# Performance work log

Measured on AMD Instinct MI355X. Metric: run time of the kernel, lower is better.

Reference implementation:

```python
import jax, jax.numpy as jnp
import numpy as np

NUM_HEADS = 16
EMBED = 1024
N, S = 4, 2048


def setup_inputs() -> dict:
    key = jax.random.key(0)
    k1, k2, k3, k4, k5 = jax.random.split(key, 5)
    return {
        "values": jax.random.normal(k1, (N, S, EMBED), dtype=jnp.float32),
        "keys": jax.random.normal(k2, (N, S, EMBED), dtype=jnp.float32),
        "query": jax.random.normal(k3, (N, S, EMBED), dtype=jnp.float32),
        "mask": jnp.ones((N, 1, 1, S), dtype=jnp.int32),
        "W_out": jax.random.normal(k4, (EMBED, EMBED), dtype=jnp.float32) * 0.02,
        "b_out": jax.random.normal(k5, (EMBED,), dtype=jnp.float32) * 0.02,
    }


def reference(values, keys, query, mask, W_out, b_out):
    n, q_len, e = query.shape
    h = NUM_HEADS
    d = e // h
    v = values.reshape(n, -1, h, d)   # [N, K, H, D]
    k = keys.reshape(n, -1, h, d)     # [N, K, H, D]
    q = query.reshape(n, q_len, h, d) # [N, Q, H, D]
    # [N, H, Q, K] similarity (full materialization, as in source)
    sim = jnp.einsum('nqhd,nkhd->nhqk', q, k)
    sim = jnp.where(mask == 0, -jnp.inf, sim)
    # NOTE: source scales by sqrt(embed_size), not sqrt(head_dim)
    attn = jax.nn.softmax(sim / jnp.sqrt(jnp.float32(e)), axis=3)
    out = jnp.einsum('nhqk,nkhd->nqhd', attn, v).reshape(n, q_len, e)
    return out @ W_out.T + b_out
```

## Files before the change

kernel.cpp:

```cpp
#include <hip/hip_runtime.h>

#define SEQ 2048
#define EMBED 1024
#define NHEADS 16
#define HD 64

typedef __attribute__((ext_vector_type(4))) float f32x4;
typedef __attribute__((ext_vector_type(16))) float f32x16;
typedef __attribute__((ext_vector_type(8))) unsigned short u16x8;
typedef __attribute__((ext_vector_type(8))) __bf16 bf16x8;

static __device__ __forceinline__ unsigned cvtpk(float a, float b) {
  unsigned r;
  asm("v_cvt_pk_bf16_f32 %0, %1, %2" : "=v"(r) : "v"(a), "v"(b));
  return r;
}

static __device__ __forceinline__ f32x4 mfma16(u16x8 a, u16x8 b, f32x4 c) {
  return __builtin_amdgcn_mfma_f32_16x16x32_bf16(
      __builtin_bit_cast(bf16x8, a), __builtin_bit_cast(bf16x8, b), c, 0, 0, 0);
}

static __device__ __forceinline__ f32x16 mfma32(u16x8 a, u16x8 b, f32x16 c) {
  return __builtin_amdgcn_mfma_f32_32x32x16_bf16(
      __builtin_bit_cast(bf16x8, a), __builtin_bit_cast(bf16x8, b), c, 0, 0, 0);
}

static __device__ __forceinline__ void gload_lds16(const void* g, void* l) {
  __builtin_amdgcn_global_load_lds(
      (const __attribute__((address_space(1))) unsigned*)g,
      (__attribute__((address_space(3))) unsigned*)l, 16, 0, 0);
}

static __device__ __forceinline__ f32x16 zero16() {
  f32x16 z;
#pragma unroll
  for (int i = 0; i < 16; ++i) z[i] = 0.f;
  return z;
}

static __device__ __forceinline__ u16x8 packfrag(float p0, float p1, float p2, float p3,
                                                 float p4, float p5, float p6, float p7) {
  unsigned L0 = cvtpk(p0, p1);
  unsigned L1 = cvtpk(p2, p3);
  unsigned M0 = cvtpk(p4, p5);
  unsigned M1 = cvtpk(p6, p7);
  asm volatile("v_permlane32_swap_b32 %0, %1" : "+v"(L0), "+v"(M0));
  asm volatile("v_permlane32_swap_b32 %0, %1" : "+v"(L1), "+v"(M1));
  const uint4 fr = make_uint4(L0, L1, M0, M1);
  return __builtin_bit_cast(u16x8, fr);
}

__global__ void convw(const float* __restrict__ W, unsigned short* __restrict__ Wb) {
  const int i = (blockIdx.x * 256 + threadIdx.x) * 4;
  f32x4 v = *(const f32x4*)(W + i);
  *(uint2*)&Wb[i] = make_uint2(cvtpk(v[0], v[1]), cvtpk(v[2], v[3]));
}

__global__ __launch_bounds__(256) void convkv(const float* __restrict__ Kg,
                                              const float* __restrict__ Vg,
                                              unsigned short* __restrict__ Kb,
                                              unsigned short* __restrict__ Vt) {
  const int t = threadIdx.x;
  const int kb = blockIdx.x, nh = blockIdx.y;
  const int n = nh >> 4, h = nh & 15;

  {
    const int k = t >> 2;
    const int ks = t & 3;
    const float* src = Kg + (size_t)(n * SEQ + kb * 64 + k) * EMBED + h * HD + ks * 16;
    f32x4 a = *(const f32x4*)(src);
    f32x4 b = *(const f32x4*)(src + 4);
    f32x4 c = *(const f32x4*)(src + 8);
    f32x4 d = *(const f32x4*)(src + 12);
    unsigned short* dst = Kb + ((size_t)nh * 32 + kb) * 4096 + ks * 1024 + k * 16;
    *(uint4*)&dst[0] =
        make_uint4(cvtpk(a[0], a[1]), cvtpk(a[2], a[3]), cvtpk(b[0], b[1]), cvtpk(b[2], b[3]));
    *(uint4*)&dst[8] =
        make_uint4(cvtpk(c[0], c[1]), cvtpk(c[2], c[3]), cvtpk(d[0], d[1]), cvtpk(d[2], d[3]));
  }

  {
    const int kq = t >> 4, dq = t & 15;
    const int d0 = dq * 4;
    f32x4 vv[4];
#pragma unroll
    for (int i = 0; i < 4; ++i)
      vv[i] = *(const f32x4*)(Vg + (size_t)(n * SEQ + kb * 64 + 4 * kq + i) * EMBED +
                              h * HD + d0);
    unsigned short* dst =
        Vt + ((size_t)nh * 32 + kb) * 4096 + (kq >> 1) * 512 + 4 * (kq & 1);
#pragma unroll
    for (int dj = 0; dj < 4; ++dj) {
      const int d = d0 + dj;
      *(uint2*)&dst[d * 8] =
          make_uint2(cvtpk(vv[0][dj], vv[1][dj]), cvtpk(vv[2][dj], vv[3][dj]));
    }
  }
}

__global__ __launch_bounds__(256, 2) void attn_fused(
    const unsigned short* __restrict__ Kb, const unsigned short* __restrict__ Vtb,
    const float* __restrict__ Qg, const int* __restrict__ maskg,
    unsigned short* __restrict__ attn_out)
{
  __shared__ __align__(16) unsigned short smem[16384];

  const int tid = threadIdx.x;
  const int w = tid >> 6;
  const int l = tid & 63;
  const int q = l & 31;
  const int hi = l >> 5;
  const int id = blockIdx.x;
  const int nh = (id & 7) * 8 + ((id >> 3) & 7);
  const int qb = id >> 6;
  const int n = nh >> 4, h = nh & 15;

  const unsigned short* ksrc = Kb + (size_t)nh * 32 * 4096;
  const unsigned short* vsrc = Vtb + (size_t)nh * 32 * 4096;

  {
    const unsigned short* kg = ksrc + tid * 8;
    const unsigned short* vg = vsrc + tid * 8;
    gload_lds16(kg, &smem[tid * 8]); gload_lds16(kg + 2048, &smem[tid * 8 + 2048]);
    gload_lds16(vg, &smem[8192 + tid * 8]); gload_lds16(vg + 2048, &smem[8192 + tid * 8 + 2048]);
  }

  const float C = 0.04508422f;
  u16x8 qfA[4], qfB[4];
  {
    const float* qp =
        Qg + (size_t)(n * SEQ + qb * 256 + w * 64 + q) * EMBED + h * HD + hi * 8;
#pragma unroll
    for (int ks = 0; ks < 4; ++ks) {
      f32x4 a = *(const f32x4*)(qp + ks * 16);
      f32x4 b = *(const f32x4*)(qp + ks * 16 + 4);
      uint4 pk = make_uint4(cvtpk(a[0] * C, a[1] * C), cvtpk(a[2] * C, a[3] * C),
                            cvtpk(b[0] * C, b[1] * C), cvtpk(b[2] * C, b[3] * C));
      qfA[ks] = __builtin_bit_cast(u16x8, pk);
      f32x4 a2 = *(const f32x4*)(qp + 32 * EMBED + ks * 16);
      f32x4 b2 = *(const f32x4*)(qp + 32 * EMBED + ks * 16 + 4);
      uint4 pk2 = make_uint4(cvtpk(a2[0] * C, a2[1] * C), cvtpk(a2[2] * C, a2[3] * C),
                             cvtpk(b2[0] * C, b2[1] * C), cvtpk(b2[2] * C, b2[3] * C));
      qfB[ks] = __builtin_bit_cast(u16x8, pk2);
    }
  }

  const uint4 onesu = make_uint4(0x3F803F80u, 0x3F803F80u, 0x3F803F80u, 0x3F803F80u);
  const u16x8 ones = __builtin_bit_cast(u16x8, onesu);

  f32x16 o0A = zero16(), o1A = zero16(), o0B = zero16(), o1B = zero16();
  f32x16 laccA = zero16(), laccB = zero16();
  const int kA = q * 16 + hi * 8;
  const int vA = q * 8 + hi * 512;

#pragma unroll 1
  for (int kb = 0; kb < 32; ++kb) {
    const int kbase = (kb & 1) << 12;
    const int vbase = 8192 + kbase;
    const int mv = maskg[n * SEQ + kb * 64 + l];
    __syncthreads();
    if (kb < 31) {
      const unsigned short* kg = ksrc + (size_t)(kb + 1) * 4096 + tid * 8;
      const unsigned short* vg = vsrc + (size_t)(kb + 1) * 4096 + tid * 8;
      const int ob = ((kb + 1) & 1) << 12;
      gload_lds16(kg, &smem[ob + tid * 8]);
      gload_lds16(kg + 2048, &smem[ob + tid * 8 + 2048]);
      gload_lds16(vg, &smem[8192 + ob + tid * 8]);
      gload_lds16(vg + 2048, &smem[8192 + ob + tid * 8 + 2048]);
    }
    const bool anym = __any(mv == 0);

    f32x16 sA0 = zero16(), sA1 = zero16(), sB0 = zero16(), sB1 = zero16();
    __builtin_amdgcn_s_setprio(1);
#pragma unroll
    for (int ks = 0; ks < 4; ++ks) {
      u16x8 k0 = *(const u16x8*)&smem[kbase + ks * 1024 + kA];
      sA0 = mfma32(k0, qfA[ks], sA0);
      sB0 = mfma32(k0, qfB[ks], sB0);
      u16x8 k1 = *(const u16x8*)&smem[kbase + ks * 1024 + kA + 512];
      sA1 = mfma32(k1, qfA[ks], sA1);
      sB1 = mfma32(k1, qfB[ks], sB1);
    }
    __builtin_amdgcn_s_setprio(0);

    if (anym) {
#pragma unroll
      for (int r = 0; r < 16; ++r) {
        const int kl = (r & 3) + 8 * (r >> 2) + 4 * hi;
        const float b0 = maskg[n * SEQ + kb * 64 + kl] ? 0.f : -1e5f;
        const float b1 = maskg[n * SEQ + kb * 64 + kl + 32] ? 0.f : -1e5f;
        sA0[r] += b0; sB0[r] += b0;
        sA1[r] += b1; sB1[r] += b1;
      }
    }

#pragma unroll
    for (int r = 0; r < 16; ++r) {
      sA0[r] = __builtin_amdgcn_exp2f(sA0[r]);
      sA1[r] = __builtin_amdgcn_exp2f(sA1[r]);
      sB0[r] = __builtin_amdgcn_exp2f(sB0[r]);
      sB1[r] = __builtin_amdgcn_exp2f(sB1[r]);
    }

    u16x8 paA[4], paB[4];
    paA[0] = packfrag(sA0[0], sA0[1], sA0[2], sA0[3], sA0[4], sA0[5], sA0[6], sA0[7]);
    paA[1] = packfrag(sA0[8], sA0[9], sA0[10], sA0[11], sA0[12], sA0[13], sA0[14], sA0[15]);
    paA[2] = packfrag(sA1[0], sA1[1], sA1[2], sA1[3], sA1[4], sA1[5], sA1[6], sA1[7]);
    paA[3] = packfrag(sA1[8], sA1[9], sA1[10], sA1[11], sA1[12], sA1[13], sA1[14], sA1[15]);
    paB[0] = packfrag(sB0[0], sB0[1], sB0[2], sB0[3], sB0[4], sB0[5], sB0[6], sB0[7]);
    paB[1] = packfrag(sB0[8], sB0[9], sB0[10], sB0[11], sB0[12], sB0[13], sB0[14], sB0[15]);
    paB[2] = packfrag(sB1[0], sB1[1], sB1[2], sB1[3], sB1[4], sB1[5], sB1[6], sB1[7]);
    paB[3] = packfrag(sB1[8], sB1[9], sB1[10], sB1[11], sB1[12], sB1[13], sB1[14], sB1[15]);

    __builtin_amdgcn_s_setprio(1);
#pragma unroll
    for (int idx = 0; idx < 4; ++idx) {
      u16x8 v0 = *(const u16x8*)&smem[vbase + idx * 1024 + vA];
      o0A = mfma32(v0, paA[idx], o0A);
      o0B = mfma32(v0, paB[idx], o0B);
      u16x8 v1 = *(const u16x8*)&smem[vbase + idx * 1024 + vA + 256];
      o1A = mfma32(v1, paA[idx], o1A);
      o1B = mfma32(v1, paB[idx], o1B);
      laccA = mfma32(ones, paA[idx], laccA);
      laccB = mfma32(ones, paB[idx], laccB);
    }
    __builtin_amdgcn_s_setprio(0);
  }

  const float invA = 1.f / laccA[0];
  const float invB = 1.f / laccB[0];
  __syncthreads();
  unsigned short* ep = &smem[w * 2304];
  const size_t orow = (size_t)n * SEQ + qb * 256 + w * 64;

#pragma unroll
  for (int u = 0; u < 4; ++u) {
    *(uint2*)&ep[q * 72 + 8 * u + 4 * hi] =
        make_uint2(cvtpk(o0A[4 * u] * invA, o0A[4 * u + 1] * invA),
                   cvtpk(o0A[4 * u + 2] * invA, o0A[4 * u + 3] * invA));
    *(uint2*)&ep[q * 72 + 8 * u + 4 * hi + 32] =
        make_uint2(cvtpk(o1A[4 * u] * invA, o1A[4 * u + 1] * invA),
                   cvtpk(o1A[4 * u + 2] * invA, o1A[4 * u + 3] * invA));
  }
  asm volatile("s_waitcnt lgkmcnt(0)" ::: "memory");
#pragma unroll
  for (int i = 0; i < 4; ++i) {
    const int q2 = i * 8 + (l >> 3);
    const uint4 vv = *(const uint4*)&ep[q2 * 72 + (l & 7) * 8];
    *(uint4*)&attn_out[(orow + q2) * EMBED + h * HD + (l & 7) * 8] = vv;
  }
  asm volatile("s_waitcnt lgkmcnt(0)" ::: "memory");

#pragma unroll
  for (int u = 0; u < 4; ++u) {
    *(uint2*)&ep[q * 72 + 8 * u + 4 * hi] =
        make_uint2(cvtpk(o0B[4 * u] * invB, o0B[4 * u + 1] * invB),
                   cvtpk(o0B[4 * u + 2] * invB, o0B[4 * u + 3] * invB));
    *(uint2*)&ep[q * 72 + 8 * u + 4 * hi + 32] =
        make_uint2(cvtpk(o1B[4 * u] * invB, o1B[4 * u + 1] * invB),
                   cvtpk(o1B[4 * u + 2] * invB, o1B[4 * u + 3] * invB));
  }
  asm volatile("s_waitcnt lgkmcnt(0)" ::: "memory");
#pragma unroll
  for (int i = 0; i < 4; ++i) {
    const int q2 = i * 8 + (l >> 3);
    const uint4 vv = *(const uint4*)&ep[q2 * 72 + (l & 7) * 8];
    *(uint4*)&attn_out[(orow + 32 + q2) * EMBED + h * HD + (l & 7) * 8] = vv;
  }
}

__global__ __launch_bounds__(256, 2) void proj_gemm(
    const unsigned short* __restrict__ A, const unsigned short* __restrict__ Bw,
    const float* __restrict__ bias, float* __restrict__ out)
{
  __shared__ __align__(16) unsigned short As[128 * 64];
  __shared__ __align__(16) unsigned short Bs[128 * 64];
  const int tid = threadIdx.x;
  const int l = tid & 63, m = l & 15, g = l >> 4;
  const int w = tid >> 6, wm = w >> 1, wn = w & 1;
  const int m0 = blockIdx.y * 128, n0 = blockIdx.x * 128;
  const int srow = tid >> 3, slot = tid & 7;

  f32x4 acc[4][4];
#pragma unroll
  for (int i = 0; i < 4; ++i)
#pragma unroll
    for (int j = 0; j < 4; ++j) acc[i][j] = (f32x4){0.f, 0.f, 0.f, 0.f};

  for (int kk = 0; kk < EMBED; kk += 64) {
    __syncthreads();
#pragma unroll
    for (int i = 0; i < 4; ++i) {
      const int row = i * 32 + srow;
      u16x8 va = *(const u16x8*)(A + (size_t)(m0 + row) * EMBED + kk + slot * 8);
      u16x8 vb = *(const u16x8*)(Bw + (size_t)(n0 + row) * EMBED + kk + slot * 8);
      const int soff = (slot * 8) ^ ((row & 7) << 3);
      *(u16x8*)&As[row * 64 + soff] = va;
      *(u16x8*)&Bs[row * 64 + soff] = vb;
    }
    __syncthreads();
#pragma unroll
    for (int kc = 0; kc < 2; ++kc) {
      u16x8 af[4], bf[4];
#pragma unroll
      for (int mi = 0; mi < 4; ++mi) {
        const int row = wm * 64 + mi * 16 + m;
        af[mi] = *(const u16x8*)&As[row * 64 + ((kc * 32 + g * 8) ^ ((row & 7) << 3))];
      }
#pragma unroll
      for (int ni = 0; ni < 4; ++ni) {
        const int row = wn * 64 + ni * 16 + m;
        bf[ni] = *(const u16x8*)&Bs[row * 64 + ((kc * 32 + g * 8) ^ ((row & 7) << 3))];
      }
#pragma unroll
      for (int mi = 0; mi < 4; ++mi)
#pragma unroll
        for (int ni = 0; ni < 4; ++ni)
          acc[mi][ni] = mfma16(af[mi], bf[ni], acc[mi][ni]);
    }
  }

#pragma unroll
  for (int ni = 0; ni < 4; ++ni) {
    const int col = n0 + wn * 64 + ni * 16 + m;
    const float bv = bias[col];
#pragma unroll
    for (int mi = 0; mi < 4; ++mi) {
      const int rb = m0 + wm * 64 + mi * 16 + g * 4;
#pragma unroll
      for (int r = 0; r < 4; ++r)
        out[(size_t)(rb + r) * EMBED + col] = acc[mi][ni][r] + bv;
    }
  }
}

extern "C" void kernel_launch(void* const* d_in, const int* in_sizes, int n_in,
                              void* d_out, int out_size, void* d_ws, size_t ws_size,
                              hipStream_t stream) {
  const float* Vg = (const float*)d_in[0];
  const float* Kg = (const float*)d_in[1];
  const float* Qg = (const float*)d_in[2];
  const int* maskg = (const int*)d_in[3];
  const float* Wg = (const float*)d_in[4];
  const float* bg = (const float*)d_in[5];

  unsigned short* attn = (unsigned short*)d_ws;
  unsigned short* Wb = attn + (size_t)4 * SEQ * EMBED;
  unsigned short* Kb = Wb + (size_t)EMBED * EMBED;
  unsigned short* Vt = Kb + (size_t)4 * SEQ * EMBED;
  float* out = (float*)d_out;

  convw<<<dim3(EMBED * EMBED / 1024), 256, 0, stream>>>(Wg, Wb);
  convkv<<<dim3(SEQ / 64, 4 * NHEADS), 256, 0, stream>>>(Kg, Vg, Kb, Vt);
  attn_fused<<<dim3(512), 256, 0, stream>>>(Kb, Vt, Qg, maskg, attn);
  proj_gemm<<<dim3(EMBED / 128, 4 * SEQ / 128), 256, 0, stream>>>(attn, Wb, bg, out);
}
```

Baseline: 130.4 us.

## Fuse weight conversion into KV conversion, precompute mask bias in LDS, tighten loop barriers

```diff
diff --git a/kernel.cpp b/kernel.cpp
--- a/kernel.cpp
+++ b/kernel.cpp
@@ -51,16 +51,12 @@
   return __builtin_bit_cast(u16x8, fr);
 }
 
-__global__ void convw(const float* __restrict__ W, unsigned short* __restrict__ Wb) {
-  const int i = (blockIdx.x * 256 + threadIdx.x) * 4;
-  f32x4 v = *(const f32x4*)(W + i);
-  *(uint2*)&Wb[i] = make_uint2(cvtpk(v[0], v[1]), cvtpk(v[2], v[3]));
-}
-
 __global__ __launch_bounds__(256) void convkv(const float* __restrict__ Kg,
                                               const float* __restrict__ Vg,
+                                              const float* __restrict__ Wg,
                                               unsigned short* __restrict__ Kb,
-                                              unsigned short* __restrict__ Vt) {
+                                              unsigned short* __restrict__ Vt,
+                                              unsigned short* __restrict__ Wb) {
   const int t = threadIdx.x;
   const int kb = blockIdx.x, nh = blockIdx.y;
   const int n = nh >> 4, h = nh & 15;
@@ -97,6 +93,12 @@
           make_uint2(cvtpk(vv[0][dj], vv[1][dj]), cvtpk(vv[2][dj], vv[3][dj]));
     }
   }
+
+  {
+    const int bid = blockIdx.y * 32 + blockIdx.x;
+    const float2 wv = *(const float2*)&Wg[(size_t)bid * 512 + t * 2];
+    ((unsigned*)Wb)[(size_t)bid * 256 + t] = cvtpk(wv.x, wv.y);
+  }
 }
 
 __global__ __launch_bounds__(256, 2) void attn_fused(
@@ -105,6 +107,8 @@
     unsigned short* __restrict__ attn_out)
 {
   __shared__ __align__(16) unsigned short smem[16384];
+  __shared__ float bias_lds[2048];
+  __shared__ int maskflag;
 
   const int tid = threadIdx.x;
   const int w = tid >> 6;
@@ -118,6 +122,24 @@
 
   const unsigned short* ksrc = Kb + (size_t)nh * 32 * 4096;
   const unsigned short* vsrc = Vtb + (size_t)nh * 32 * 4096;
+
+  if (tid == 0) maskflag = 0;
+  const int4 m4a = *(const int4*)&maskg[n * SEQ + tid * 8];
+  const int4 m4b = *(const int4*)&maskg[n * SEQ + tid * 8 + 4];
+  bias_lds[tid * 8 + 0] = m4a.x ? 0.f : -1e5f;
+  bias_lds[tid * 8 + 1] = m4a.y ? 0.f : -1e5f;
+  bias_lds[tid * 8 + 2] = m4a.z ? 0.f : -1e5f;
+  bias_lds[tid * 8 + 3] = m4a.w ? 0.f : -1e5f;
+  bias_lds[tid * 8 + 4] = m4b.x ? 0.f : -1e5f;
+  bias_lds[tid * 8 + 5] = m4b.y ? 0.f : -1e5f;
+  bias_lds[tid * 8 + 6] = m4b.z ? 0.f : -1e5f;
+  bias_lds[tid * 8 + 7] = m4b.w ? 0.f : -1e5f;
+  __syncthreads();
+  if ((m4a.x == 0) || (m4a.y == 0) || (m4a.z == 0) || (m4a.w == 0) ||
+      (m4b.x == 0) || (m4b.y == 0) || (m4b.z == 0) || (m4b.w == 0))
+    maskflag = 1;
+  __syncthreads();
+  const bool anyz = (maskflag != 0);
 
   {
     const unsigned short* kg = ksrc + tid * 8;
@@ -158,8 +180,6 @@
   for (int kb = 0; kb < 32; ++kb) {
     const int kbase = (kb & 1) << 12;
     const int vbase = 8192 + kbase;
-    const int mv = maskg[n * SEQ + kb * 64 + l];
-    __syncthreads();
     if (kb < 31) {
       const unsigned short* kg = ksrc + (size_t)(kb + 1) * 4096 + tid * 8;
       const unsigned short* vg = vsrc + (size_t)(kb + 1) * 4096 + tid * 8;
@@ -168,8 +188,13 @@
       gload_lds16(kg + 2048, &smem[ob + tid * 8 + 2048]);
       gload_lds16(vg, &smem[8192 + ob + tid * 8]);
       gload_lds16(vg + 2048, &smem[8192 + ob + tid * 8 + 2048]);
-    }
-    const bool anym = __any(mv == 0);
+      asm volatile("s_waitcnt vmcnt(4)" ::: "memory");
+    } else {
+      asm volatile("s_waitcnt vmcnt(0)" ::: "memory");
+    }
+    __builtin_amdgcn_sched_barrier(0);
+    __builtin_amdgcn_s_barrier();
+    __builtin_amdgcn_sched_barrier(0);
 
     f32x16 sA0 = zero16(), sA1 = zero16(), sB0 = zero16(), sB1 = zero16();
     __builtin_amdgcn_s_setprio(1);
@@ -184,12 +209,12 @@
     }
     __builtin_amdgcn_s_setprio(0);
 
-    if (anym) {
+    if (anyz) {
 #pragma unroll
       for (int r = 0; r < 16; ++r) {
         const int kl = (r & 3) + 8 * (r >> 2) + 4 * hi;
-        const float b0 = maskg[n * SEQ + kb * 64 + kl] ? 0.f : -1e5f;
-        const float b1 = maskg[n * SEQ + kb * 64 + kl + 32] ? 0.f : -1e5f;
+        const float b0 = bias_lds[kb * 64 + kl];
+        const float b1 = bias_lds[kb * 64 + kl + 32];
         sA0[r] += b0; sB0[r] += b0;
         sA1[r] += b1; sB1[r] += b1;
       }
@@ -226,6 +251,9 @@
       laccB = mfma32(ones, paB[idx], laccB);
     }
     __builtin_amdgcn_s_setprio(0);
+
+    __builtin_amdgcn_sched_barrier(0);
+    __builtin_amdgcn_s_barrier();
   }
 
   const float invA = 1.f / laccA[0];
@@ -351,8 +379,7 @@
   unsigned short* Vt = Kb + (size_t)4 * SEQ * EMBED;
   float* out = (float*)d_out;
 
-  convw<<<dim3(EMBED * EMBED / 1024), 256, 0, stream>>>(Wg, Wb);
-  convkv<<<dim3(SEQ / 64, 4 * NHEADS), 256, 0, stream>>>(Kg, Vg, Kb, Vt);
+  convkv<<<dim3(SEQ / 64, 4 * NHEADS), 256, 0, stream>>>(Kg, Vg, Wg, Kb, Vt, Wb);
   attn_fused<<<dim3(512), 256, 0, stream>>>(Kb, Vt, Qg, maskg, attn);
   proj_gemm<<<dim3(EMBED / 128, 4 * SEQ / 128), 256, 0, stream>>>(attn, Wb, bg, out);
 }
```

Result: faster. 125.0 us (-4.1%).
